# Performance work log

Hardware: AMD Instinct MI355X
Metric: run time of the kernel (lower is better)

The kernel has to match this reference:

```python
import jax, jax.numpy as jnp
import numpy as np

V, E, LD, NLANG, H, B, T = 8000, 150, 50, 10, 512, 100, 50
D0 = E + LD  # layer-0 GRU input size


def setup_inputs() -> dict:
    key = jax.random.key(0)
    ks = jax.random.split(key, 12)
    iw = 0.5 / E  # TF init_width
    def rn(k, shape, s=0.05):
        return jax.random.normal(k, shape, jnp.float32) * s
    return {
        "input_data": jax.random.randint(ks[0], (B, T), 0, V, jnp.int32),
        "langs": jax.random.randint(ks[1], (B,), 0, NLANG, jnp.int32),
        "targets": jax.random.randint(ks[2], (B, T), 0, V, jnp.int32),
        "embedding": jax.random.uniform(ks[3], (V, E), jnp.float32, -iw, iw),
        "lang_emb": jax.random.uniform(ks[4], (NLANG, LD), jnp.float32, -iw, iw),
        "Wg0": rn(ks[5], (D0 + H, 2 * H)),
        "bg0": jnp.ones((2 * H,), jnp.float32),  # TF GRUCell bias_start=1.0
        "Wc0": rn(ks[6], (D0 + H, H)),
        "bc0": jnp.zeros((H,), jnp.float32),
        "Wg1": rn(ks[7], (H + H, 2 * H)),
        "bg1": jnp.ones((2 * H,), jnp.float32),
        "Wc1": rn(ks[8], (H + H, H)),
        "bc1": jnp.zeros((H,), jnp.float32),
        "softmax_w": rn(ks[9], (H, V)),
        "softmax_b": jnp.zeros((V,), jnp.float32),
    }


def _l2norm(x):
    return x / jnp.sqrt(jnp.maximum(jnp.sum(x * x, axis=1, keepdims=True), 1e-12))


def _gru(h, x, Wg, bg, Wc, bc):
    # TF GRUCell: r,u = sigmoid([x,h]Wg + bg); c = tanh([x, r*h]Wc + bc)
    ru = jax.nn.sigmoid(jnp.concatenate([x, h], axis=1) @ Wg + bg)
    r, u = jnp.split(ru, 2, axis=1)
    c = jnp.tanh(jnp.concatenate([x, r * h], axis=1) @ Wc + bc)
    return u * h + (1.0 - u) * c


def reference(input_data, langs, targets, embedding, lang_emb,
              Wg0, bg0, Wc0, bc0, Wg1, bg1, Wc1, bc1, softmax_w, softmax_b):
    emb = _l2norm(embedding)[input_data]          # [B,T,E]
    lg = _l2norm(lang_emb)[langs]                 # [B,LD]
    lg = jnp.broadcast_to(lg[:, None, :], (B, T, LD))
    xs = jnp.concatenate([emb, lg], axis=-1)      # [B,T,D0]
    xs = jnp.transpose(xs, (1, 0, 2))             # [T,B,D0]

    def step(carry, x_t):
        h0, h1 = carry
        h0 = _gru(h0, x_t, Wg0, bg0, Wc0, bc0)
        h1 = _gru(h1, h0, Wg1, bg1, Wc1, bc1)
        return (h0, h1), h1

    init = (jnp.zeros((B, H), xs.dtype), jnp.zeros((B, H), xs.dtype))
    _, outs = jax.lax.scan(step, init, xs)        # [T,B,H]
    output = jnp.transpose(outs, (1, 0, 2)).reshape(B * T, H)
    logits = output @ softmax_w + softmax_b       # [B*T,V]
    logp = jax.nn.log_softmax(logits, axis=-1)
    nll = -jnp.take_along_axis(logp, targets.reshape(-1, 1), axis=1)[:, 0]
    cost = jnp.sum(nll) / (B * T)
    return cost
```

## Files before the change

kernel.cpp:

```cpp
#include <hip/hip_runtime.h>
#include <hip/hip_bf16.h>
#include <hip/hip_fp8.h>
#include <math.h>

#define V_    8000
#define E_    150
#define LD_   50
#define H_    512
#define B_    100
#define T_    50
#define D0_   200
#define BT_   5000
#define NV_   8000
#define KXP_  224

typedef __attribute__((ext_vector_type(8))) short short8v;
typedef __attribute__((ext_vector_type(4))) float f32x4;
typedef __attribute__((ext_vector_type(2))) long long2v;

__device__ __forceinline__ float sigmoidf_(float x) { return 1.0f / (1.0f + expf(-x)); }
__device__ __forceinline__ unsigned short f2b(float x) {
    __hip_bfloat16 b = __float2bfloat16(x);
    return *(unsigned short*)&b;
}
__device__ __forceinline__ unsigned char f2e4(float x) {
    __hip_fp8_e4m3 v(x);
    return (unsigned char)v.__x;
}
__device__ __forceinline__ void gload16(const void* g, void* l) {
    __builtin_amdgcn_global_load_lds(
        (__attribute__((address_space(1))) void*)(g),
        (__attribute__((address_space(3))) void*)(l), 16, 0, 0);
}

__global__ __launch_bounds__(256) void norm_rows(const float* __restrict__ in,
                                                 float* __restrict__ out, int R, int C) {
    int row = blockIdx.x;
    if (row >= R) return;
    int tid = threadIdx.x;
    float v = (tid < C) ? in[(size_t)row * C + tid] : 0.f;
    __shared__ float red[256];
    red[tid] = v * v;
    __syncthreads();
    for (int s = 128; s > 0; s >>= 1) {
        if (tid < s) red[tid] += red[tid + s];
        __syncthreads();
    }
    float scale = rsqrtf(fmaxf(red[0], 1e-12f));
    if (tid < C) out[(size_t)row * C + tid] = v * scale;
}

__global__ void build_xsb(const int* __restrict__ inp, const int* __restrict__ langs,
                          const float* __restrict__ nemb, const float* __restrict__ nlang,
                          unsigned short* __restrict__ xsb) {
    int idx = blockIdx.x * 256 + threadIdx.x;
    if (idx >= BT_ * KXP_) return;
    int m = idx / KXP_, e = idx % KXP_;
    int b = m % 100, t = m / 100;
    float v = 0.f;
    if (e < E_)       v = nemb[(size_t)inp[b * T_ + t] * E_ + e];
    else if (e < D0_) v = nlang[(size_t)langs[b] * LD_ + (e - E_)];
    xsb[idx] = f2b(v);
}

__global__ __launch_bounds__(256) void pack_frags(const float* __restrict__ W, int ldw,
                                                  int k0off, int KT, int NT,
                                                  unsigned short* __restrict__ dst, int klim) {
    int idx = blockIdx.x * 256 + threadIdx.x;
    if (idx >= KT * NT * 64) return;
    int lane = idx & 63;
    int tile = idx >> 6;
    int nt = tile % NT, kt = tile / NT;
    int n = nt * 16 + (lane & 15);
    int kb = k0off + kt * 32 + (lane >> 4) * 8;
    unsigned short o[8];
#pragma unroll
    for (int j = 0; j < 8; ++j)
        o[j] = (kb + j < klim) ? f2b(W[(size_t)(kb + j) * ldw + n]) : 0;
    *(uint4*)(dst + (size_t)idx * 8) = *(const uint4*)o;
}

__global__ __launch_bounds__(256) void pack_frags8(const float* __restrict__ W, int ldw,
                                                   int k0off, int KT, int NT,
                                                   unsigned char* __restrict__ dst,
                                                   float scale) {
    int idx = blockIdx.x * 256 + threadIdx.x;
    if (idx >= KT * NT * 64) return;
    int lane = idx & 63;
    int tile = idx >> 6;
    int nt = tile % NT, kt = tile / NT;
    int n = nt * 16 + (lane & 15);
    int kb = k0off + kt * 32 + (lane >> 4) * 8;
    unsigned char o[8];
#pragma unroll
    for (int j = 0; j < 8; ++j) o[j] = f2e4(W[(size_t)(kb + j) * ldw + n] * scale);
    size_t off = ((((size_t)(kt >> 1) * NT + nt) * 64 + lane) << 4) + ((kt & 1) << 3);
    *(unsigned long long*)(dst + off) = *(const unsigned long long*)o;
}

template<int NSUB, int SPK>
__device__ __forceinline__ void mm_sub(const unsigned char* gsrc0, int NT,
                                       const unsigned char* a0, unsigned char* wst,
                                       int laneoff, int aoffB, f32x4* acc) {
    const size_t gstride = (size_t)NT * 1024;
#pragma unroll
    for (int s = 0; s < 3; ++s) {
        const int ktp = (SPK == 2) ? (s >> 1) : s;
        const int h = (SPK == 2) ? (s & 1) : 0;
        const unsigned char* g = gsrc0 + (size_t)ktp * gstride + h * 2048;
        gload16(g, wst + (s & 3) * 2048);
        gload16(g + 1024, wst + (s & 3) * 2048 + 1024);
    }
    __builtin_amdgcn_sched_barrier(0);
#pragma unroll
    for (int s = 0; s < NSUB; ++s) {
        if (s + 3 < NSUB) {
            const int s3 = s + 3;
            const int ktp3 = (SPK == 2) ? (s3 >> 1) : s3;
            const int h3 = (SPK == 2) ? (s3 & 1) : 0;
            const unsigned char* g = gsrc0 + (size_t)ktp3 * gstride + h3 * 2048;
            gload16(g, wst + (s3 & 3) * 2048);
            gload16(g + 1024, wst + (s3 & 3) * 2048 + 1024);
            __builtin_amdgcn_sched_barrier(0);
        }
        {
            const int newer = (NSUB - 1 - s) < 3 ? (NSUB - 1 - s) : 3;
            if (newer == 3)      asm volatile("s_waitcnt vmcnt(6)" ::: "memory");
            else if (newer == 2) asm volatile("s_waitcnt vmcnt(4)" ::: "memory");
            else if (newer == 1) asm volatile("s_waitcnt vmcnt(2)" ::: "memory");
            else                 asm volatile("s_waitcnt vmcnt(0)" ::: "memory");
        }
        __builtin_amdgcn_sched_barrier(0);
        const int ktp = (SPK == 2) ? (s >> 1) : s;
        const int h = (SPK == 2) ? (s & 1) : 0;
        long av0 = *(const long*)(a0 + aoffB + (2 * ktp) * 32);
        long av1 = *(const long*)(a0 + aoffB + (2 * ktp + 1) * 32);
        const unsigned char* lb = wst + (s & 3) * 2048;
        long2v bv0 = *(const long2v*)(lb + laneoff);
        long2v bv1 = *(const long2v*)(lb + 1024 + laneoff);
        acc[h * 2 + 0] = __builtin_amdgcn_mfma_f32_16x16x32_fp8_fp8(av0, bv0.x, acc[h * 2 + 0], 0, 0, 0);
        acc[h * 2 + 0] = __builtin_amdgcn_mfma_f32_16x16x32_fp8_fp8(av1, bv0.y, acc[h * 2 + 0], 0, 0, 0);
        acc[h * 2 + 1] = __builtin_amdgcn_mfma_f32_16x16x32_fp8_fp8(av0, bv1.x, acc[h * 2 + 1], 0, 0, 0);
        acc[h * 2 + 1] = __builtin_amdgcn_mfma_f32_16x16x32_fp8_fp8(av1, bv1.y, acc[h * 2 + 1], 0, 0, 0);
        asm volatile("s_waitcnt lgkmcnt(0)" ::: "memory");
        __builtin_amdgcn_sched_barrier(0);
    }
}

#define INV512_ 0.001953125f
__global__ __launch_bounds__(1024) void rnn_pass8(
    const float* __restrict__ Xg, const float* __restrict__ Xc,
    const unsigned char* __restrict__ Wgf, const unsigned char* __restrict__ Wcf,
    unsigned short* __restrict__ houtb) {
    __shared__ __align__(16) unsigned char hb8[16 * 520];
    __shared__ __align__(16) unsigned char rhb8[16 * 520];
    __shared__ float hf[2 * 512], uf[2 * 512];
    __shared__ __align__(16) unsigned char wstage[16 * 8192];
    const int tid = threadIdx.x;
    const int w = tid >> 6, lane = tid & 63;
    const int arow = lane & 15;
    const int laneoff = lane * 16;
    const int aoffB = arow * 520 + (lane >> 4) * 8;
    const int rb = blockIdx.x * 2;
    unsigned char* wst = wstage + (w << 13);
    const unsigned char* gA = Wgf + ((size_t)(w * 4) * 64) * 16 + laneoff;
    const unsigned char* gB = Wcf + ((size_t)(w * 2) * 64) * 16 + laneoff;

    for (int i = tid; i < 16 * 520; i += 1024) { hb8[i] = 0; rhb8[i] = 0; }
    for (int i = tid; i < 2 * 512; i += 1024) hf[i] = 0.f;
    __syncthreads();

    for (int t = 0; t < T_; ++t) {
        const int m0 = t * 100 + rb, m1 = m0 + 1;
        {
            float xg0v[4], xg1v[4];
            if (lane < 16) {
#pragma unroll
                for (int nt = 0; nt < 4; ++nt) {
                    int col = (w * 4 + nt) * 16 + arow;
                    xg0v[nt] = Xg[(size_t)m0 * 1024 + col];
                    xg1v[nt] = Xg[(size_t)m1 * 1024 + col];
                }
            }
            __builtin_amdgcn_sched_barrier(0);
            f32x4 acc[4];
#pragma unroll
            for (int nt = 0; nt < 4; ++nt) acc[nt] = (f32x4){0.f, 0.f, 0.f, 0.f};
            mm_sub<16, 2>(gA, 64, hb8, wst, laneoff, aoffB, acc);
            if (lane < 16) {
#pragma unroll
                for (int nt = 0; nt < 4; ++nt) {
                    int col = (w * 4 + nt) * 16 + arow;
                    float s0 = sigmoidf_(fmaf(acc[nt][0], INV512_, xg0v[nt]));
                    float s1 = sigmoidf_(fmaf(acc[nt][1], INV512_, xg1v[nt]));
                    if (col < 512) {
                        rhb8[col]       = f2e4(16.f * s0 * hf[col]);
                        rhb8[520 + col] = f2e4(16.f * s1 * hf[512 + col]);
                    } else {
                        uf[col - 512] = s0;
                        uf[col]       = s1;
                    }
                }
            }
        }
        __syncthreads();
        {
            float xc0v[2], xc1v[2];
            if (lane < 16) {
#pragma unroll
                for (int nt = 0; nt < 2; ++nt) {
                    int col = (w * 2 + nt) * 16 + arow;
                    xc0v[nt] = Xc[(size_t)m0 * 512 + col];
                    xc1v[nt] = Xc[(size_t)m1 * 512 + col];
                }
            }
            __builtin_amdgcn_sched_barrier(0);
            f32x4 acc[2];
#pragma unroll
            for (int nt = 0; nt < 2; ++nt) acc[nt] = (f32x4){0.f, 0.f, 0.f, 0.f};
            mm_sub<8, 1>(gB, 32, rhb8, wst, laneoff, aoffB, acc);
            if (lane < 16) {
#pragma unroll
                for (int nt = 0; nt < 2; ++nt) {
                    int col = (w * 2 + nt) * 16 + arow;
                    float c0 = tanhf(fmaf(acc[nt][0], INV512_, xc0v[nt]));
                    float c1 = tanhf(fmaf(acc[nt][1], INV512_, xc1v[nt]));
                    float uA = uf[col], uB = uf[512 + col];
                    float hA = uA * hf[col] + (1.f - uA) * c0;
                    float hB = uB * hf[512 + col] + (1.f - uB) * c1;
                    hf[col] = hA; hf[512 + col] = hB;
                    hb8[col] = f2e4(16.f * hA); hb8[520 + col] = f2e4(16.f * hB);
                    houtb[(size_t)m0 * 512 + col] = f2b(hA);
                    houtb[(size_t)m1 * 512 + col] = f2b(hB);
                }
            }
        }
        __syncthreads();
    }
}

template<int NTW, int KT, int LDA>
__global__ __launch_bounds__(256) void xproj_mfma(const unsigned short* __restrict__ Abf,
                                                  const unsigned short* __restrict__ Wf,
                                                  const float* __restrict__ bias,
                                                  float* __restrict__ C, int M) {
    const int NT = NTW * 4;
    const int N = NT * 16;
    const int tid = threadIdx.x;
    const int w = tid >> 6, lane = tid & 63;
    const int arow = lane & 15, hi = lane >> 4;
    const int mbase = blockIdx.x * 16;
    int ga = mbase + arow; if (ga >= M) ga = M - 1;
    const unsigned short* ap = Abf + (size_t)ga * LDA + hi * 8;
    f32x4 acc[NTW];
#pragma unroll
    for (int nt = 0; nt < NTW; ++nt) acc[nt] = (f32x4){0.f, 0.f, 0.f, 0.f};
#pragma unroll 2
    for (int kt = 0; kt < KT; ++kt) {
        short8v af = *(const short8v*)(ap + kt * 32);
        const unsigned short* wp = Wf + ((size_t)(kt * NT + w * NTW) * 64 + lane) * 8;
#pragma unroll
        for (int nt = 0; nt < NTW; ++nt) {
            short8v bf = *(const short8v*)(wp + (size_t)nt * 512);
            acc[nt] = __builtin_amdgcn_mfma_f32_16x16x32_bf16(af, bf, acc[nt], 0, 0, 0);
        }
    }
#pragma unroll
    for (int nt = 0; nt < NTW; ++nt) {
        int col = (w * NTW + nt) * 16 + arow;
        float bb = bias[col];
#pragma unroll
        for (int q = 0; q < 4; ++q) {
            int gm = mbase + hi * 4 + q;
            if (gm < M) C[(size_t)gm * N + col] = acc[nt][q] + bb;
        }
    }
}

__global__ __launch_bounds__(256) void lse_mfma(const unsigned short* __restrict__ Abf,
                                                const unsigned short* __restrict__ swf,
                                                const float* __restrict__ sb,
                                                const int* __restrict__ tgt,
                                                float* __restrict__ zt,
                                                float* __restrict__ parts) {
    const int tid = threadIdx.x;
    const int w = tid >> 6, lane = tid & 63;
    const int arow = lane & 15, hi = lane >> 4;
    const int mbase = blockIdx.y * 64 + w * 16;
    const int ntg0 = blockIdx.x * 4;
    int ga = mbase + arow; if (ga >= BT_) ga = BT_ - 1;
    const unsigned short* ap = Abf + (size_t)ga * 512 + hi * 8;
    f32x4 acc[4];
#pragma unroll
    for (int nt = 0; nt < 4; ++nt) acc[nt] = (f32x4){0.f, 0.f, 0.f, 0.f};
#pragma unroll 2
    for (int kt = 0; kt < 16; ++kt) {
        short8v af = *(const short8v*)(ap + kt * 32);
        const unsigned short* wp = swf + ((size_t)(kt * 500 + ntg0) * 64 + lane) * 8;
#pragma unroll
        for (int nt = 0; nt < 4; ++nt) {
            short8v bf = *(const short8v*)(wp + (size_t)nt * 512);
            acc[nt] = __builtin_amdgcn_mfma_f32_16x16x32_bf16(af, bf, acc[nt], 0, 0, 0);
        }
    }
#pragma unroll
    for (int nt = 0; nt < 4; ++nt) {
        float bb = sb[(ntg0 + nt) * 16 + arow];
#pragma unroll
        for (int q = 0; q < 4; ++q) acc[nt][q] += bb;
    }
#pragma unroll
    for (int q = 0; q < 4; ++q) {
        int gr = mbase + hi * 4 + q;
        if (gr < BT_) {
            int tg = tgt[(gr % 100) * 50 + gr / 100];
            int lt = tg - arow;
#pragma unroll
            for (int nt = 0; nt < 4; ++nt)
                if (lt == (ntg0 + nt) * 16) zt[gr] = acc[nt][q];
        }
    }
    float lm[4], ls[4];
#pragma unroll
    for (int q = 0; q < 4; ++q)
        lm[q] = fmaxf(fmaxf(acc[0][q], acc[1][q]), fmaxf(acc[2][q], acc[3][q]));
#pragma unroll
    for (int mask = 1; mask < 16; mask <<= 1)
#pragma unroll
        for (int q = 0; q < 4; ++q) lm[q] = fmaxf(lm[q], __shfl_xor(lm[q], mask));
#pragma unroll
    for (int q = 0; q < 4; ++q) {
        float s = 0.f;
#pragma unroll
        for (int nt = 0; nt < 4; ++nt) s += expf(acc[nt][q] - lm[q]);
        ls[q] = s;
    }
#pragma unroll
    for (int mask = 1; mask < 16; mask <<= 1)
#pragma unroll
        for (int q = 0; q < 4; ++q) ls[q] += __shfl_xor(ls[q], mask);
    if (arow == 0) {
#pragma unroll
        for (int q = 0; q < 4; ++q) {
            int gr = mbase + hi * 4 + q;
            if (gr < BT_) {
                parts[(size_t)gr * 250 + blockIdx.x * 2 + 0] = lm[q];
                parts[(size_t)gr * 250 + blockIdx.x * 2 + 1] = ls[q];
            }
        }
    }
}

__global__ __launch_bounds__(128) void final_nll(const float* __restrict__ parts,
                                                 const float* __restrict__ zt,
                                                 float* __restrict__ bsum) {
    int i = blockIdx.x * 128 + threadIdx.x;
    float nll = 0.f;
    if (i < BT_) {
        const float* p = parts + (size_t)i * 250;
        float M = p[0];
        for (int j = 1; j < 125; ++j) M = fmaxf(M, p[2 * j]);
        float S = 0.f;
        for (int j = 0; j < 125; ++j) S += p[2 * j + 1] * expf(p[2 * j] - M);
        nll = M + logf(S) - zt[i];
    }
    __shared__ float red[128];
    red[threadIdx.x] = nll;
    __syncthreads();
    for (int s = 64; s > 0; s >>= 1) {
        if (threadIdx.x < s) red[threadIdx.x] += red[threadIdx.x + s];
        __syncthreads();
    }
    if (threadIdx.x == 0) bsum[blockIdx.x] = red[0];
}

__global__ __launch_bounds__(64) void final_sum(const float* __restrict__ bsum,
                                                float* __restrict__ out) {
    int tid = threadIdx.x;
    float v = (tid < 40) ? bsum[tid] : 0.f;
    for (int off = 32; off > 0; off >>= 1) v += __shfl_down(v, off);
    if (tid == 0) out[0] = v / 5000.0f;
}

extern "C" void kernel_launch(void* const* d_in, const int* in_sizes, int n_in,
                              void* d_out, int out_size, void* d_ws, size_t ws_size,
                              hipStream_t stream) {
    const int*   inp   = (const int*)d_in[0];
    const int*   langs = (const int*)d_in[1];
    const int*   tgt   = (const int*)d_in[2];
    const float* emb   = (const float*)d_in[3];
    const float* lemb  = (const float*)d_in[4];
    const float* Wg0   = (const float*)d_in[5];
    const float* bg0   = (const float*)d_in[6];
    const float* Wc0   = (const float*)d_in[7];
    const float* bc0   = (const float*)d_in[8];
    const float* Wg1   = (const float*)d_in[9];
    const float* bg1   = (const float*)d_in[10];
    const float* Wc1   = (const float*)d_in[11];
    const float* bc1   = (const float*)d_in[12];
    const float* sw    = (const float*)d_in[13];
    const float* sb    = (const float*)d_in[14];
    float* out = (float*)d_out;

    float* w = (float*)d_ws;
    float* nemb = w;
    unsigned char* a8 = (unsigned char*)w;
    unsigned char* Wg0f8  = a8;
    unsigned char* Wc0f8  = a8 + 524288;
    unsigned char* Wg1hf8 = a8 + 786432;
    unsigned char* Wc1hf8 = a8 + 1310720;
    unsigned short* Wg1xf = (unsigned short*)(a8 + 1572864);
    unsigned short* Wc1xf = Wg1xf + 524288;
    float* nlang = w + 1200000;
    unsigned short* xsb   = (unsigned short*)(w + 1200512);
    unsigned short* Wg0xf = (unsigned short*)(w + 1760512);
    unsigned short* Wc0xf = (unsigned short*)(w + 1875200);
    float* Xg0   = w + 2200512;
    float* Xg1   = w + 2200512;
    unsigned short* swf = (unsigned short*)(w + 2200512);
    float* Xc0   = w + 7320512;
    float* Xc1   = w + 7320512;
    float* parts = w + 7320512;
    float* ztb   = w + 7320512 + 1250000;
    float* bsum  = w + 7320512 + 1255000;
    unsigned short* h0seq = (unsigned short*)(w + 9880512);
    unsigned short* h1o   = (unsigned short*)(w + 9880512);

    norm_rows<<<V_, 256, 0, stream>>>(emb, nemb, V_, E_);
    norm_rows<<<10, 256, 0, stream>>>(lemb, nlang, 10, LD_);
    build_xsb<<<(BT_ * KXP_ + 255) / 256, 256, 0, stream>>>(inp, langs, nemb, nlang, xsb);
    pack_frags8<<<256, 256, 0, stream>>>(Wg0, 1024, D0_, 16, 64, Wg0f8, 32.f);
    pack_frags8<<<128, 256, 0, stream>>>(Wc0,  512, D0_, 16, 32, Wc0f8, 32.f);
    pack_frags8<<<256, 256, 0, stream>>>(Wg1, 1024, 512, 16, 64, Wg1hf8, 32.f);
    pack_frags8<<<128, 256, 0, stream>>>(Wc1,  512, 512, 16, 32, Wc1hf8, 32.f);
    pack_frags<<<256, 256, 0, stream>>>(Wg1, 1024, 0, 16, 64, Wg1xf, 1 << 30);
    pack_frags<<<128, 256, 0, stream>>>(Wc1,  512, 0, 16, 32, Wc1xf, 1 << 30);
    pack_frags<<<112, 256, 0, stream>>>(Wg0, 1024, 0, 7, 64, Wg0xf, D0_);
    pack_frags<<<56, 256, 0, stream>>>(Wc0,  512, 0, 7, 32, Wc0xf, D0_);
    xproj_mfma<16, 7, KXP_><<<313, 256, 0, stream>>>(xsb, Wg0xf, bg0, Xg0, BT_);
    xproj_mfma<8, 7, KXP_><<<313, 256, 0, stream>>>(xsb, Wc0xf, bc0, Xc0, BT_);
    rnn_pass8<<<50, 1024, 0, stream>>>(Xg0, Xc0, Wg0f8, Wc0f8, h0seq);
    xproj_mfma<16, 16, 512><<<313, 256, 0, stream>>>(h0seq, Wg1xf, bg1, Xg1, BT_);
    xproj_mfma<8, 16, 512><<<313, 256, 0, stream>>>(h0seq, Wc1xf, bc1, Xc1, BT_);
    rnn_pass8<<<50, 1024, 0, stream>>>(Xg1, Xc1, Wg1hf8, Wc1hf8, h1o);
    pack_frags<<<2000, 256, 0, stream>>>(sw, NV_, 0, 16, 500, swf, 1 << 30);
    lse_mfma<<<dim3(125, 79), 256, 0, stream>>>(h1o, swf, sb, tgt, ztb, parts);
    final_nll<<<40, 128, 0, stream>>>(parts, ztb, bsum);
    final_sum<<<1, 64, 0, stream>>>(bsum, out);
}
```

Before: 1.676 ms.

## Pipeline weight streaming across gate and candidate phases with rotated K order

Replaces the per-phase mm_sub helper with an inline double-buffered loop that prefetches the next phase's weight tiles while the current phase computes, so weight fetch latency is not exposed at each phase start. The K-chunk order is rotated by block index so concurrent blocks hit different weight regions, spreading L2 traffic. Xg/Xc loads move into the middle of the loop, and __syncthreads becomes an explicit lgkmcnt wait plus s_barrier so outstanding global prefetches can stay in flight across the barrier. The hand-counted vmcnt values are fragile, and a wrong count would read stale LDS data.

```diff
diff --git a/kernel.cpp b/kernel.cpp
--- a/kernel.cpp
+++ b/kernel.cpp
@@ -96,55 +96,6 @@
     for (int j = 0; j < 8; ++j) o[j] = f2e4(W[(size_t)(kb + j) * ldw + n] * scale);
     size_t off = ((((size_t)(kt >> 1) * NT + nt) * 64 + lane) << 4) + ((kt & 1) << 3);
     *(unsigned long long*)(dst + off) = *(const unsigned long long*)o;
-}
-
-template<int NSUB, int SPK>
-__device__ __forceinline__ void mm_sub(const unsigned char* gsrc0, int NT,
-                                       const unsigned char* a0, unsigned char* wst,
-                                       int laneoff, int aoffB, f32x4* acc) {
-    const size_t gstride = (size_t)NT * 1024;
-#pragma unroll
-    for (int s = 0; s < 3; ++s) {
-        const int ktp = (SPK == 2) ? (s >> 1) : s;
-        const int h = (SPK == 2) ? (s & 1) : 0;
-        const unsigned char* g = gsrc0 + (size_t)ktp * gstride + h * 2048;
-        gload16(g, wst + (s & 3) * 2048);
-        gload16(g + 1024, wst + (s & 3) * 2048 + 1024);
-    }
-    __builtin_amdgcn_sched_barrier(0);
-#pragma unroll
-    for (int s = 0; s < NSUB; ++s) {
-        if (s + 3 < NSUB) {
-            const int s3 = s + 3;
-            const int ktp3 = (SPK == 2) ? (s3 >> 1) : s3;
-            const int h3 = (SPK == 2) ? (s3 & 1) : 0;
-            const unsigned char* g = gsrc0 + (size_t)ktp3 * gstride + h3 * 2048;
-            gload16(g, wst + (s3 & 3) * 2048);
-            gload16(g + 1024, wst + (s3 & 3) * 2048 + 1024);
-            __builtin_amdgcn_sched_barrier(0);
-        }
-        {
-            const int newer = (NSUB - 1 - s) < 3 ? (NSUB - 1 - s) : 3;
-            if (newer == 3)      asm volatile("s_waitcnt vmcnt(6)" ::: "memory");
-            else if (newer == 2) asm volatile("s_waitcnt vmcnt(4)" ::: "memory");
-            else if (newer == 1) asm volatile("s_waitcnt vmcnt(2)" ::: "memory");
-            else                 asm volatile("s_waitcnt vmcnt(0)" ::: "memory");
-        }
-        __builtin_amdgcn_sched_barrier(0);
-        const int ktp = (SPK == 2) ? (s >> 1) : s;
-        const int h = (SPK == 2) ? (s & 1) : 0;
-        long av0 = *(const long*)(a0 + aoffB + (2 * ktp) * 32);
-        long av1 = *(const long*)(a0 + aoffB + (2 * ktp + 1) * 32);
-        const unsigned char* lb = wst + (s & 3) * 2048;
-        long2v bv0 = *(const long2v*)(lb + laneoff);
-        long2v bv1 = *(const long2v*)(lb + 1024 + laneoff);
-        acc[h * 2 + 0] = __builtin_amdgcn_mfma_f32_16x16x32_fp8_fp8(av0, bv0.x, acc[h * 2 + 0], 0, 0, 0);
-        acc[h * 2 + 0] = __builtin_amdgcn_mfma_f32_16x16x32_fp8_fp8(av1, bv0.y, acc[h * 2 + 0], 0, 0, 0);
-        acc[h * 2 + 1] = __builtin_amdgcn_mfma_f32_16x16x32_fp8_fp8(av0, bv1.x, acc[h * 2 + 1], 0, 0, 0);
-        acc[h * 2 + 1] = __builtin_amdgcn_mfma_f32_16x16x32_fp8_fp8(av1, bv1.y, acc[h * 2 + 1], 0, 0, 0);
-        asm volatile("s_waitcnt lgkmcnt(0)" ::: "memory");
-        __builtin_amdgcn_sched_barrier(0);
-    }
 }
 
 #define INV512_ 0.001953125f
@@ -162,31 +113,76 @@
     const int laneoff = lane * 16;
     const int aoffB = arow * 520 + (lane >> 4) * 8;
     const int rb = blockIdx.x * 2;
+    const int rot = blockIdx.x & 7;
     unsigned char* wst = wstage + (w << 13);
     const unsigned char* gA = Wgf + ((size_t)(w * 4) * 64) * 16 + laneoff;
     const unsigned char* gB = Wcf + ((size_t)(w * 2) * 64) * 16 + laneoff;
+    const size_t gsA = 64 * 1024;
+    const size_t gsB = 32 * 1024;
 
     for (int i = tid; i < 16 * 520; i += 1024) { hb8[i] = 0; rhb8[i] = 0; }
     for (int i = tid; i < 2 * 512; i += 1024) hf[i] = 0.f;
     __syncthreads();
+
+#pragma unroll
+    for (int nt = 0; nt < 4; ++nt)
+        gload16(gA + (size_t)rot * gsA + nt * 1024, wst + nt * 1024);
+    __builtin_amdgcn_sched_barrier(0);
+#pragma unroll
+    for (int nt = 0; nt < 4; ++nt)
+        gload16(gA + (size_t)((rot + 1) & 7) * gsA + nt * 1024, wst + 4096 + nt * 1024);
+    __builtin_amdgcn_sched_barrier(0);
 
     for (int t = 0; t < T_; ++t) {
         const int m0 = t * 100 + rb, m1 = m0 + 1;
         {
             float xg0v[4], xg1v[4];
-            if (lane < 16) {
+            f32x4 acc[4];
+#pragma unroll
+            for (int nt = 0; nt < 4; ++nt) acc[nt] = (f32x4){0.f, 0.f, 0.f, 0.f};
+#pragma unroll
+            for (int i = 0; i < 8; ++i) {
+                const int g = (rot + i) & 7;
+                if (i == 3 || i == 4) asm volatile("s_waitcnt vmcnt(12)" ::: "memory");
+                else if (i == 7)      asm volatile("s_waitcnt vmcnt(2)" ::: "memory");
+                else                  asm volatile("s_waitcnt vmcnt(4)" ::: "memory");
+                __builtin_amdgcn_sched_barrier(0);
+                unsigned char* lb = wst + (i & 1) * 4096;
+                long av0 = *(const long*)(hb8 + aoffB + (2 * g) * 32);
+                long av1 = *(const long*)(hb8 + aoffB + (2 * g + 1) * 32);
 #pragma unroll
                 for (int nt = 0; nt < 4; ++nt) {
-                    int col = (w * 4 + nt) * 16 + arow;
-                    xg0v[nt] = Xg[(size_t)m0 * 1024 + col];
-                    xg1v[nt] = Xg[(size_t)m1 * 1024 + col];
+                    long2v bv = *(const long2v*)(lb + nt * 1024 + laneoff);
+                    acc[nt] = __builtin_amdgcn_mfma_f32_16x16x32_fp8_fp8(av0, bv.x, acc[nt], 0, 0, 0);
+                    acc[nt] = __builtin_amdgcn_mfma_f32_16x16x32_fp8_fp8(av1, bv.y, acc[nt], 0, 0, 0);
+                }
+                __builtin_amdgcn_sched_barrier(0);
+                if (i < 6) {
+                    const int g2 = (rot + i + 2) & 7;
+#pragma unroll
+                    for (int nt = 0; nt < 4; ++nt)
+                        gload16(gA + (size_t)g2 * gsA + nt * 1024, lb + nt * 1024);
+                } else if (i == 6) {
+                    gload16(gB + (size_t)rot * gsB, wst);
+                    gload16(gB + (size_t)rot * gsB + 1024, wst + 1024);
+                } else {
+                    const int gb = (rot + 1) & 7;
+                    gload16(gB + (size_t)gb * gsB, wst + 4096);
+                    gload16(gB + (size_t)gb * gsB + 1024, wst + 4096 + 1024);
+                }
+                __builtin_amdgcn_sched_barrier(0);
+                if (i == 2) {
+                    if (lane < 16) {
+#pragma unroll
+                        for (int nt = 0; nt < 4; ++nt) {
+                            int col = (w * 4 + nt) * 16 + arow;
+                            xg0v[nt] = Xg[(size_t)m0 * 1024 + col];
+                            xg1v[nt] = Xg[(size_t)m1 * 1024 + col];
+                        }
+                    }
+                    __builtin_amdgcn_sched_barrier(0);
                 }
             }
-            __builtin_amdgcn_sched_barrier(0);
-            f32x4 acc[4];
-#pragma unroll
-            for (int nt = 0; nt < 4; ++nt) acc[nt] = (f32x4){0.f, 0.f, 0.f, 0.f};
-            mm_sub<16, 2>(gA, 64, hb8, wst, laneoff, aoffB, acc);
             if (lane < 16) {
 #pragma unroll
                 for (int nt = 0; nt < 4; ++nt) {
@@ -203,22 +199,58 @@
                 }
             }
         }
-        __syncthreads();
+        asm volatile("s_waitcnt lgkmcnt(0)" ::: "memory");
+        __builtin_amdgcn_s_barrier();
         {
             float xc0v[2], xc1v[2];
-            if (lane < 16) {
+            f32x4 acc[2];
+#pragma unroll
+            for (int nt = 0; nt < 2; ++nt) acc[nt] = (f32x4){0.f, 0.f, 0.f, 0.f};
+#pragma unroll
+            for (int i = 0; i < 8; ++i) {
+                const int g = (rot + i) & 7;
+                if (i == 3 || i == 4) asm volatile("s_waitcnt vmcnt(6)" ::: "memory");
+                else if (i == 7)      asm volatile("s_waitcnt vmcnt(4)" ::: "memory");
+                else                  asm volatile("s_waitcnt vmcnt(2)" ::: "memory");
+                __builtin_amdgcn_sched_barrier(0);
+                unsigned char* lb = wst + (i & 1) * 4096;
+                long av0 = *(const long*)(rhb8 + aoffB + (2 * g) * 32);
+                long av1 = *(const long*)(rhb8 + aoffB + (2 * g + 1) * 32);
 #pragma unroll
                 for (int nt = 0; nt < 2; ++nt) {
-                    int col = (w * 2 + nt) * 16 + arow;
-                    xc0v[nt] = Xc[(size_t)m0 * 512 + col];
-                    xc1v[nt] = Xc[(size_t)m1 * 512 + col];
+                    long2v bv = *(const long2v*)(lb + nt * 1024 + laneoff);
+                    acc[nt] = __builtin_amdgcn_mfma_f32_16x16x32_fp8_fp8(av0, bv.x, acc[nt], 0, 0, 0);
+                    acc[nt] = __builtin_amdgcn_mfma_f32_16x16x32_fp8_fp8(av1, bv.y, acc[nt], 0, 0, 0);
+                }
+                __builtin_amdgcn_sched_barrier(0);
+                if (i < 6) {
+                    const int g2 = (rot + i + 2) & 7;
+#pragma unroll
+                    for (int nt = 0; nt < 2; ++nt)
+                        gload16(gB + (size_t)g2 * gsB + nt * 1024, lb + nt * 1024);
+                } else if (i == 6) {
+#pragma unroll
+                    for (int nt = 0; nt < 4; ++nt)
+                        gload16(gA + (size_t)rot * gsA + nt * 1024, wst + nt * 1024);
+                } else {
+                    const int ga1 = (rot + 1) & 7;
+#pragma unroll
+                    for (int nt = 0; nt < 4; ++nt)
+                        gload16(gA + (size_t)ga1 * gsA + nt * 1024, wst + 4096 + nt * 1024);
+                }
+                __builtin_amdgcn_sched_barrier(0);
+                if (i == 2) {
+                    if (lane < 16) {
+#pragma unroll
+                        for (int nt = 0; nt < 2; ++nt) {
+                            int col = (w * 2 + nt) * 16 + arow;
+                            xc0v[nt] = Xc[(size_t)m0 * 512 + col];
+                            xc1v[nt] = Xc[(size_t)m1 * 512 + col];
+                        }
+                    }
+                    __builtin_amdgcn_sched_barrier(0);
                 }
             }
-            __builtin_amdgcn_sched_barrier(0);
-            f32x4 acc[2];
-#pragma unroll
-            for (int nt = 0; nt < 2; ++nt) acc[nt] = (f32x4){0.f, 0.f, 0.f, 0.f};
-            mm_sub<8, 1>(gB, 32, rhb8, wst, laneoff, aoffB, acc);
             if (lane < 16) {
 #pragma unroll
                 for (int nt = 0; nt < 2; ++nt) {
@@ -235,7 +267,8 @@
                 }
             }
         }
-        __syncthreads();
+        asm volatile("s_waitcnt lgkmcnt(0)" ::: "memory");
+        __builtin_amdgcn_s_barrier();
     }
 }
 
```

New measurement: 1.648 ms. About the same (-1.7%).

## Restructure recurrent fp8 matmul pipeline and merge small setup kernels

Applied to the files above, without the earlier changes.

The weight-streaming loop in the recurrent GRU kernel is reorganized so that each stage loads all N-tiles for one K-pair at once and double-buffers two K-pairs ahead, replacing the previous 3-deep sub-tile ring. It also drops the per-step lgkmcnt wait. Separately, the two normalization launches are merged into one kernel and the eight weight-packing launches into a single pack_all kernel, which cuts launch overhead. The new pipeline issues bigger batches of loads per stage but has a shallower prefetch depth in stage count, so latency hiding could change.

```diff
diff --git a/kernel.cpp b/kernel.cpp
--- a/kernel.cpp
+++ b/kernel.cpp
@@ -33,10 +33,14 @@
         (__attribute__((address_space(3))) void*)(l), 16, 0, 0);
 }
 
-__global__ __launch_bounds__(256) void norm_rows(const float* __restrict__ in,
-                                                 float* __restrict__ out, int R, int C) {
-    int row = blockIdx.x;
-    if (row >= R) return;
+__global__ __launch_bounds__(256) void norm_both(const float* __restrict__ emb,
+                                                 const float* __restrict__ lemb,
+                                                 float* __restrict__ nemb,
+                                                 float* __restrict__ nlang) {
+    int b = blockIdx.x;
+    const float* in; float* out; int row, C;
+    if (b < V_) { in = emb; out = nemb; row = b; C = E_; }
+    else        { in = lemb; out = nlang; row = b - V_; C = LD_; }
     int tid = threadIdx.x;
     float v = (tid < C) ? in[(size_t)row * C + tid] : 0.f;
     __shared__ float red[256];
@@ -63,11 +67,9 @@
     xsb[idx] = f2b(v);
 }
 
-__global__ __launch_bounds__(256) void pack_frags(const float* __restrict__ W, int ldw,
-                                                  int k0off, int KT, int NT,
-                                                  unsigned short* __restrict__ dst, int klim) {
-    int idx = blockIdx.x * 256 + threadIdx.x;
-    if (idx >= KT * NT * 64) return;
+__device__ __forceinline__ void pack_b16_dev(const float* __restrict__ W, int ldw,
+                                             int k0off, int NT, int klim,
+                                             unsigned short* __restrict__ dst, int idx) {
     int lane = idx & 63;
     int tile = idx >> 6;
     int nt = tile % NT, kt = tile / NT;
@@ -79,13 +81,9 @@
         o[j] = (kb + j < klim) ? f2b(W[(size_t)(kb + j) * ldw + n]) : 0;
     *(uint4*)(dst + (size_t)idx * 8) = *(const uint4*)o;
 }
-
-__global__ __launch_bounds__(256) void pack_frags8(const float* __restrict__ W, int ldw,
-                                                   int k0off, int KT, int NT,
-                                                   unsigned char* __restrict__ dst,
-                                                   float scale) {
-    int idx = blockIdx.x * 256 + threadIdx.x;
-    if (idx >= KT * NT * 64) return;
+__device__ __forceinline__ void pack_f8_dev(const float* __restrict__ W, int ldw,
+                                            int k0off, int NT,
+                                            unsigned char* __restrict__ dst, int idx) {
     int lane = idx & 63;
     int tile = idx >> 6;
     int nt = tile % NT, kt = tile / NT;
@@ -93,57 +91,74 @@
     int kb = k0off + kt * 32 + (lane >> 4) * 8;
     unsigned char o[8];
 #pragma unroll
-    for (int j = 0; j < 8; ++j) o[j] = f2e4(W[(size_t)(kb + j) * ldw + n] * scale);
+    for (int j = 0; j < 8; ++j) o[j] = f2e4(W[(size_t)(kb + j) * ldw + n] * 32.f);
     size_t off = ((((size_t)(kt >> 1) * NT + nt) * 64 + lane) << 4) + ((kt & 1) << 3);
     *(unsigned long long*)(dst + off) = *(const unsigned long long*)o;
 }
 
-template<int NSUB, int SPK>
-__device__ __forceinline__ void mm_sub(const unsigned char* gsrc0, int NT,
-                                       const unsigned char* a0, unsigned char* wst,
-                                       int laneoff, int aoffB, f32x4* acc) {
+__global__ __launch_bounds__(256) void pack_all(
+    const float* __restrict__ Wg0, const float* __restrict__ Wc0,
+    const float* __restrict__ Wg1, const float* __restrict__ Wc1,
+    unsigned char* __restrict__ Wg0f8, unsigned char* __restrict__ Wc0f8,
+    unsigned char* __restrict__ Wg1hf8, unsigned char* __restrict__ Wc1hf8,
+    unsigned short* __restrict__ Wg1xf, unsigned short* __restrict__ Wc1xf,
+    unsigned short* __restrict__ Wg0xf, unsigned short* __restrict__ Wc0xf) {
+    int b = blockIdx.x, tid = threadIdx.x;
+    if (b < 256)        pack_f8_dev(Wg0, 1024, D0_, 64, Wg0f8, b * 256 + tid);
+    else if (b < 384)   pack_f8_dev(Wc0,  512, D0_, 32, Wc0f8, (b - 256) * 256 + tid);
+    else if (b < 640)   pack_f8_dev(Wg1, 1024, 512, 64, Wg1hf8, (b - 384) * 256 + tid);
+    else if (b < 768)   pack_f8_dev(Wc1,  512, 512, 32, Wc1hf8, (b - 640) * 256 + tid);
+    else if (b < 1024)  pack_b16_dev(Wg1, 1024, 0, 64, 1 << 30, Wg1xf, (b - 768) * 256 + tid);
+    else if (b < 1152)  pack_b16_dev(Wc1,  512, 0, 32, 1 << 30, Wc1xf, (b - 1024) * 256 + tid);
+    else if (b < 1264)  pack_b16_dev(Wg0, 1024, 0, 64, D0_, Wg0xf, (b - 1152) * 256 + tid);
+    else                pack_b16_dev(Wc0,  512, 0, 32, D0_, Wc0xf, (b - 1264) * 256 + tid);
+}
+
+__global__ __launch_bounds__(256) void pack_frags(const float* __restrict__ W, int ldw,
+                                                  int KT, int NT,
+                                                  unsigned short* __restrict__ dst) {
+    int idx = blockIdx.x * 256 + threadIdx.x;
+    if (idx >= KT * NT * 64) return;
+    pack_b16_dev(W, ldw, 0, NT, 1 << 30, dst, idx);
+}
+
+template<int NTW>
+__device__ __forceinline__ void mm_phase8s(const unsigned char* gsrc0, int NT,
+                                           const unsigned char* a0, unsigned char* wst,
+                                           int laneoff, int aoffB, f32x4* acc) {
     const size_t gstride = (size_t)NT * 1024;
 #pragma unroll
-    for (int s = 0; s < 3; ++s) {
-        const int ktp = (SPK == 2) ? (s >> 1) : s;
-        const int h = (SPK == 2) ? (s & 1) : 0;
-        const unsigned char* g = gsrc0 + (size_t)ktp * gstride + h * 2048;
-        gload16(g, wst + (s & 3) * 2048);
-        gload16(g + 1024, wst + (s & 3) * 2048 + 1024);
-    }
+    for (int nt = 0; nt < NTW; ++nt) gload16(gsrc0 + nt * 1024, wst + nt * 1024);
     __builtin_amdgcn_sched_barrier(0);
 #pragma unroll
-    for (int s = 0; s < NSUB; ++s) {
-        if (s + 3 < NSUB) {
-            const int s3 = s + 3;
-            const int ktp3 = (SPK == 2) ? (s3 >> 1) : s3;
-            const int h3 = (SPK == 2) ? (s3 & 1) : 0;
-            const unsigned char* g = gsrc0 + (size_t)ktp3 * gstride + h3 * 2048;
-            gload16(g, wst + (s3 & 3) * 2048);
-            gload16(g + 1024, wst + (s3 & 3) * 2048 + 1024);
-            __builtin_amdgcn_sched_barrier(0);
-        }
-        {
-            const int newer = (NSUB - 1 - s) < 3 ? (NSUB - 1 - s) : 3;
-            if (newer == 3)      asm volatile("s_waitcnt vmcnt(6)" ::: "memory");
-            else if (newer == 2) asm volatile("s_waitcnt vmcnt(4)" ::: "memory");
-            else if (newer == 1) asm volatile("s_waitcnt vmcnt(2)" ::: "memory");
-            else                 asm volatile("s_waitcnt vmcnt(0)" ::: "memory");
+    for (int nt = 0; nt < NTW; ++nt)
+        gload16(gsrc0 + gstride + nt * 1024, wst + (NTW + nt) * 1024);
+    __builtin_amdgcn_sched_barrier(0);
+#pragma unroll
+    for (int ktp = 0; ktp < 8; ++ktp) {
+        if (ktp < 7) {
+            if (NTW == 4) asm volatile("s_waitcnt vmcnt(4)" ::: "memory");
+            else          asm volatile("s_waitcnt vmcnt(2)" ::: "memory");
+        } else {
+            asm volatile("s_waitcnt vmcnt(0)" ::: "memory");
         }
         __builtin_amdgcn_sched_barrier(0);
-        const int ktp = (SPK == 2) ? (s >> 1) : s;
-        const int h = (SPK == 2) ? (s & 1) : 0;
+        unsigned char* lb = wst + (ktp & 1) * (NTW * 1024);
         long av0 = *(const long*)(a0 + aoffB + (2 * ktp) * 32);
         long av1 = *(const long*)(a0 + aoffB + (2 * ktp + 1) * 32);
-        const unsigned char* lb = wst + (s & 3) * 2048;
-        long2v bv0 = *(const long2v*)(lb + laneoff);
-        long2v bv1 = *(const long2v*)(lb + 1024 + laneoff);
-        acc[h * 2 + 0] = __builtin_amdgcn_mfma_f32_16x16x32_fp8_fp8(av0, bv0.x, acc[h * 2 + 0], 0, 0, 0);
-        acc[h * 2 + 0] = __builtin_amdgcn_mfma_f32_16x16x32_fp8_fp8(av1, bv0.y, acc[h * 2 + 0], 0, 0, 0);
-        acc[h * 2 + 1] = __builtin_amdgcn_mfma_f32_16x16x32_fp8_fp8(av0, bv1.x, acc[h * 2 + 1], 0, 0, 0);
-        acc[h * 2 + 1] = __builtin_amdgcn_mfma_f32_16x16x32_fp8_fp8(av1, bv1.y, acc[h * 2 + 1], 0, 0, 0);
-        asm volatile("s_waitcnt lgkmcnt(0)" ::: "memory");
+#pragma unroll
+        for (int nt = 0; nt < NTW; ++nt) {
+            long2v bv = *(const long2v*)(lb + nt * 1024 + laneoff);
+            acc[nt] = __builtin_amdgcn_mfma_f32_16x16x32_fp8_fp8(av0, bv.x, acc[nt], 0, 0, 0);
+            acc[nt] = __builtin_amdgcn_mfma_f32_16x16x32_fp8_fp8(av1, bv.y, acc[nt], 0, 0, 0);
+        }
         __builtin_amdgcn_sched_barrier(0);
+        if (ktp + 2 < 8) {
+#pragma unroll
+            for (int nt = 0; nt < NTW; ++nt)
+                gload16(gsrc0 + (size_t)(ktp + 2) * gstride + nt * 1024, lb + nt * 1024);
+            __builtin_amdgcn_sched_barrier(0);
+        }
     }
 }
 
@@ -186,7 +201,7 @@
             f32x4 acc[4];
 #pragma unroll
             for (int nt = 0; nt < 4; ++nt) acc[nt] = (f32x4){0.f, 0.f, 0.f, 0.f};
-            mm_sub<16, 2>(gA, 64, hb8, wst, laneoff, aoffB, acc);
+            mm_phase8s<4>(gA, 64, hb8, wst, laneoff, aoffB, acc);
             if (lane < 16) {
 #pragma unroll
                 for (int nt = 0; nt < 4; ++nt) {
@@ -218,7 +233,7 @@
             f32x4 acc[2];
 #pragma unroll
             for (int nt = 0; nt < 2; ++nt) acc[nt] = (f32x4){0.f, 0.f, 0.f, 0.f};
-            mm_sub<8, 1>(gB, 32, rhb8, wst, laneoff, aoffB, acc);
+            mm_phase8s<2>(gB, 32, rhb8, wst, laneoff, aoffB, acc);
             if (lane < 16) {
 #pragma unroll
                 for (int nt = 0; nt < 2; ++nt) {
@@ -426,24 +441,17 @@
     unsigned short* h0seq = (unsigned short*)(w + 9880512);
     unsigned short* h1o   = (unsigned short*)(w + 9880512);
 
-    norm_rows<<<V_, 256, 0, stream>>>(emb, nemb, V_, E_);
-    norm_rows<<<10, 256, 0, stream>>>(lemb, nlang, 10, LD_);
+    norm_both<<<V_ + 10, 256, 0, stream>>>(emb, lemb, nemb, nlang);
     build_xsb<<<(BT_ * KXP_ + 255) / 256, 256, 0, stream>>>(inp, langs, nemb, nlang, xsb);
-    pack_frags8<<<256, 256, 0, stream>>>(Wg0, 1024, D0_, 16, 64, Wg0f8, 32.f);
-    pack_frags8<<<128, 256, 0, stream>>>(Wc0,  512, D0_, 16, 32, Wc0f8, 32.f);
-    pack_frags8<<<256, 256, 0, stream>>>(Wg1, 1024, 512, 16, 64, Wg1hf8, 32.f);
-    pack_frags8<<<128, 256, 0, stream>>>(Wc1,  512, 512, 16, 32, Wc1hf8, 32.f);
-    pack_frags<<<256, 256, 0, stream>>>(Wg1, 1024, 0, 16, 64, Wg1xf, 1 << 30);
-    pack_frags<<<128, 256, 0, stream>>>(Wc1,  512, 0, 16, 32, Wc1xf, 1 << 30);
-    pack_frags<<<112, 256, 0, stream>>>(Wg0, 1024, 0, 7, 64, Wg0xf, D0_);
-    pack_frags<<<56, 256, 0, stream>>>(Wc0,  512, 0, 7, 32, Wc0xf, D0_);
+    pack_all<<<1320, 256, 0, stream>>>(Wg0, Wc0, Wg1, Wc1, Wg0f8, Wc0f8, Wg1hf8, Wc1hf8,
+                                       Wg1xf, Wc1xf, Wg0xf, Wc0xf);
     xproj_mfma<16, 7, KXP_><<<313, 256, 0, stream>>>(xsb, Wg0xf, bg0, Xg0, BT_);
     xproj_mfma<8, 7, KXP_><<<313, 256, 0, stream>>>(xsb, Wc0xf, bc0, Xc0, BT_);
     rnn_pass8<<<50, 1024, 0, stream>>>(Xg0, Xc0, Wg0f8, Wc0f8, h0seq);
     xproj_mfma<16, 16, 512><<<313, 256, 0, stream>>>(h0seq, Wg1xf, bg1, Xg1, BT_);
     xproj_mfma<8, 16, 512><<<313, 256, 0, stream>>>(h0seq, Wc1xf, bc1, Xc1, BT_);
     rnn_pass8<<<50, 1024, 0, stream>>>(Xg1, Xc1, Wg1hf8, Wc1hf8, h1o);
-    pack_frags<<<2000, 256, 0, stream>>>(sw, NV_, 0, 16, 500, swf, 1 << 30);
+    pack_frags<<<2000, 256, 0, stream>>>(sw, NV_, 16, 500, swf);
     lse_mfma<<<dim3(125, 79), 256, 0, stream>>>(h1o, swf, sb, tgt, ztb, parts);
     final_nll<<<40, 128, 0, stream>>>(parts, ztb, bsum);
     final_sum<<<1, 64, 0, stream>>>(bsum, out);
```

After: 1.541 ms, median of 2. -8.0%, faster.
